# Kernel tuning notes

Measured on AMD Instinct MI355X. Metric: run time of the kernel, lower is better.

The kernel has to match this reference:

```python
import jax, jax.numpy as jnp
import numpy as np

D = 128
K = 8
TEMPERATURE = 1.0
LN_EPS = 1e-5
NORM_EPS = 1e-12


def setup_inputs() -> dict:
    key = jax.random.key(0)
    ks = jax.random.split(key, 6)
    B = 262144
    global_prosody = jax.random.normal(ks[0], (B, D), dtype=jnp.float32)
    W = jax.random.normal(ks[1], (D, D), dtype=jnp.float32) / np.sqrt(D)
    b = jnp.zeros((D,), dtype=jnp.float32)
    gamma = jnp.ones((D,), dtype=jnp.float32)
    beta = jnp.zeros((D,), dtype=jnp.float32)
    # codebook initialized as rows of an orthonormal basis (SVD of random init)
    init = jax.random.normal(ks[2], (D, K), dtype=jnp.float32)
    U, _, _ = jnp.linalg.svd(init, full_matrices=False)
    codebook = U[:, :K].T  # (K, D)
    return {"global_prosody": global_prosody, "W": W, "b": b,
            "gamma": gamma, "beta": beta, "codebook": codebook}


def _l2norm(x, axis=-1):
    n = jnp.sqrt(jnp.sum(x * x, axis=axis, keepdims=True))
    return x / jnp.maximum(n, NORM_EPS)


def reference(global_prosody, W, b, gamma, beta, codebook):
    # proj: Linear + LayerNorm
    h = global_prosody @ W.T + b                      # (B, D)
    mu = jnp.mean(h, axis=-1, keepdims=True)
    var = jnp.var(h, axis=-1, keepdims=True)
    h = (h - mu) / jnp.sqrt(var + LN_EPS) * gamma + beta
    # cosine-sim logits
    h_norm = _l2norm(h)                               # (B, D)
    cb_norm = _l2norm(codebook)                       # (K, D)
    logits = (h_norm @ cb_norm.T) / TEMPERATURE       # (B, K)
    soft_assign = jax.nn.softmax(logits, axis=-1)
    hard_indices = jnp.argmax(logits, axis=-1)        # (B,)
    hard_assign = jax.nn.one_hot(hard_indices, K, dtype=jnp.float32)
    # straight-through assignment
    assign = hard_assign + soft_assign - jax.lax.stop_gradient(soft_assign)
    embedding = assign @ codebook                     # (B, D)
    return hard_indices, soft_assign, embedding, logits
```

## Files before the change

kernel.cpp:

```cpp
#include <hip/hip_runtime.h>
#include <math.h>

#define DD 128
#define KK 8
#define LN_EPS 1e-5f
#define NORM_EPS 1e-12f

typedef __attribute__((ext_vector_type(8))) short bf16x8;
typedef __attribute__((ext_vector_type(16))) float f32x16;
typedef unsigned int uint;
typedef unsigned short ushort;

#define G2B_OFF_F   (122880 / 4)
#define SCAL_OFF_F  (123904 / 4)

__device__ inline void split3(float x, uint& h, uint& m, uint& l) {
    uint u0 = __float_as_uint(x);
    uint rh = (u0 + 0x7FFFu + ((u0 >> 16) & 1u)) & 0xFFFF0000u;
    float xh = __uint_as_float(rh);
    float r1 = x - xh;
    uint u1 = __float_as_uint(r1);
    uint rm = (u1 + 0x7FFFu + ((u1 >> 16) & 1u)) & 0xFFFF0000u;
    float xm = __uint_as_float(rm);
    float r2 = r1 - xm;
    uint u2 = __float_as_uint(r2);
    uint rl = (u2 + 0x7FFFu + ((u2 >> 16) & 1u));
    h = rh; m = rm; l = rl;
}

__device__ inline void split3t(float x, uint& h, uint& m, uint& l) {
    uint u0 = __float_as_uint(x);
    float xh = __uint_as_float(u0 & 0xFFFF0000u);
    float r1 = x - xh;
    uint u1 = __float_as_uint(r1);
    float xm = __uint_as_float(u1 & 0xFFFF0000u);
    float r2 = r1 - xm;
    h = u0; m = u1; l = __float_as_uint(r2);
}

__device__ inline uint packhi(uint a1, uint a0) {
    return __builtin_amdgcn_perm(a1, a0, 0x07060302u);
}

__device__ inline void split2packt(float e0, float e1, uint& ph, uint& pm, uint& pl) {
    uint h0, m0, l0, h1, m1, l1;
    split3t(e0, h0, m0, l0);
    split3t(e1, h1, m1, l1);
    ph = packhi(h1, h0);
    pm = packhi(m1, m0);
    pl = packhi(l1, l0);
}

union FragU  { uint4 u; bf16x8 f; };
union AccU16 { f32x16 v; float a[16]; };

__global__ void l1q_prep(const float* __restrict__ W, const float* __restrict__ b,
                         const float* __restrict__ gamma, const float* __restrict__ beta,
                         const float* __restrict__ cb, ushort* __restrict__ wsA,
                         float* __restrict__ ws)
{
    __shared__ float invn_s[KK];
    __shared__ float we[11][DD];
    __shared__ float wext[32][16];
    const int t = threadIdx.x;
    const int jt = blockIdx.x >> 3;
    const int ks = blockIdx.x & 7;

    if (jt == 4) {
        if (t < KK) {
            float s = 0.f;
            for (int j = 0; j < DD; ++j) { float v = cb[t * DD + j]; s = fmaf(v, v, s); }
            invn_s[t] = 1.0f / fmaxf(sqrtf(s), NORM_EPS);
        }
        __syncthreads();
        for (int idx = t; idx < 11 * DD; idx += 256) {
            int e = idx / DD, j = idx % DD;
            float g = gamma[j];
            float v;
            if (e == 0)      v = 1.0f;
            else if (e == 1) v = g * g;
            else if (e == 2) v = g * beta[j];
            else             v = cb[(e - 3) * DD + j] * invn_s[e - 3] * g;
            we[e][j] = v;
        }
        __syncthreads();

        if (ks == 0) {
            if (t < DD) {
                float g = gamma[t];
                float* g2b = ws + G2B_OFF_F;
                g2b[2 * t]     = g * g;
                g2b[2 * t + 1] = b[t];
            }
            float* scal = ws + SCAL_OFF_F;
            if (t < KK) {
                float in = invn_s[t];
                float p = 0.f, q = 0.f, cu = 0.f;
                for (int j = 0; j < DD; ++j) {
                    float c = cb[t * DD + j] * in;
                    p  = fmaf(c, gamma[j], p);
                    q  = fmaf(c, beta[j], q);
                    cu = fmaf(c * gamma[j], b[j], cu);
                }
                scal[t]      = p;
                scal[8 + t]  = q;
                scal[22 + t] = cu;
            }
            if (t == 16) { float s = 0.f; for (int j = 0; j < DD; ++j) { float g = gamma[j]; s = fmaf(g, g, s); } scal[16] = s; }
            if (t == 17) { float s = 0.f; for (int j = 0; j < DD; ++j) s = fmaf(gamma[j], beta[j], s); scal[17] = s; }
            if (t == 18) { float s = 0.f; for (int j = 0; j < DD; ++j) { float v = beta[j]; s = fmaf(v, v, s); } scal[18] = s; }
            if (t == 19) { float s = 0.f; for (int j = 0; j < DD; ++j) s += b[j]; scal[19] = s; }
            if (t == 20) { float s = 0.f; for (int j = 0; j < DD; ++j) s = fmaf(gamma[j] * gamma[j], b[j], s); scal[20] = s; }
            if (t == 21) { float s = 0.f; for (int j = 0; j < DD; ++j) s = fmaf(gamma[j] * beta[j], b[j], s); scal[21] = s; }
        }
    }

    for (int idx = t; idx < 512; idx += 256) {
        int jl = idx >> 4, kk = idx & 15;
        int k = ks * 16 + kk;
        float val;
        if (jt < 4) {
            val = W[(jt * 32 + jl) * DD + k];
        } else if (jl < 11) {
            float s = 0.f;
            for (int j = 0; j < DD; ++j) s = fmaf(we[jl][j], W[j * DD + k], s);
            val = s;
        } else {
            val = 0.f;
        }
        wext[jl][kk] = val;
    }
    __syncthreads();

    for (int idx = t; idx < 512; idx += 256) {
        int jl = idx >> 4, kk = idx & 15;
        int lane = jl + 32 * (kk >> 3);
        int i = kk & 7;
        uint h, m, l;
        split3(wext[jl][kk], h, m, l);
        int base = jt * 8 + ks;
        wsA[(0 * 40 + base) * 512 + lane * 8 + i] = (ushort)(h >> 16);
        wsA[(1 * 40 + base) * 512 + lane * 8 + i] = (ushort)(m >> 16);
        wsA[(2 * 40 + base) * 512 + lane * 8 + i] = (ushort)(l >> 16);
    }
}

__global__ __launch_bounds__(1024, 4)
void l1q_main(const float* __restrict__ x, const ushort* __restrict__ wsA,
              const float* __restrict__ wsf, const float* __restrict__ cb,
              float* __restrict__ out_idx, float* __restrict__ out_soft,
              float* __restrict__ out_emb, float* __restrict__ out_log,
              int B)
{
    __shared__ uint4 Wl4[7680];
    __shared__ float gath[16][352];
    __shared__ int   besti[16][32];
    __shared__ float g2b_s[256];
    __shared__ float scal_s[32];

    const int t = threadIdx.x;
    const int wave = t >> 6;
    const int lane = t & 63;
    const int n = lane & 31;
    const int h = lane >> 5;
    const int rowbase = blockIdx.x * 512 + wave * 32;
    const int row = rowbase + n;

    const float* xp = x + (size_t)row * DD + h * 8;
    float4 c0a = *(const float4*)(xp + 0);
    float4 c0c = *(const float4*)(xp + 4);
    float4 c1a = *(const float4*)(xp + 16);
    float4 c1c = *(const float4*)(xp + 20);

    {
        const uint4* src = (const uint4*)wsA;
        #pragma unroll
        for (int i = 0; i < 8; ++i) {
            int idx = t + i * 1024;
            if (idx < 7680) Wl4[idx] = src[idx];
        }
    }
    if (t < 256) g2b_s[t] = wsf[G2B_OFF_F + t];
    if (t < 32)  scal_s[t] = wsf[SCAL_OFF_F + t];
    __syncthreads();

    f32x16 acc[5];
    #pragma unroll
    for (int jt = 0; jt < 5; ++jt)
        #pragma unroll
        for (int r = 0; r < 16; ++r) acc[jt][r] = 0.f;

    #pragma unroll
    for (int ks = 0; ks < 8; ++ks) {
        int kp = (ks < 6) ? ks + 2 : 7;
        float4 pa = *(const float4*)(xp + kp * 16 + 0);
        float4 pc = *(const float4*)(xp + kp * 16 + 4);

        FragU xh, xm, xl;
        split2packt(c0a.x, c0a.y, xh.u.x, xm.u.x, xl.u.x);
        split2packt(c0a.z, c0a.w, xh.u.y, xm.u.y, xl.u.y);
        split2packt(c0c.x, c0c.y, xh.u.z, xm.u.z, xl.u.z);
        split2packt(c0c.z, c0c.w, xh.u.w, xm.u.w, xl.u.w);

        #pragma unroll
        for (int jt = 0; jt < 5; ++jt) {
            const int pl = jt * 8 + ks;
            FragU wh, wm, wl;
            wh.u = Wl4[(0 * 40 + pl) * 64 + lane];
            wm.u = Wl4[(1 * 40 + pl) * 64 + lane];
            wl.u = Wl4[(2 * 40 + pl) * 64 + lane];
            f32x16 c = acc[jt];
            c = __builtin_amdgcn_mfma_f32_32x32x16_bf16(wl.f, xh.f, c, 0, 0, 0);
            c = __builtin_amdgcn_mfma_f32_32x32x16_bf16(wh.f, xl.f, c, 0, 0, 0);
            c = __builtin_amdgcn_mfma_f32_32x32x16_bf16(wm.f, xm.f, c, 0, 0, 0);
            c = __builtin_amdgcn_mfma_f32_32x32x16_bf16(wm.f, xh.f, c, 0, 0, 0);
            c = __builtin_amdgcn_mfma_f32_32x32x16_bf16(wh.f, xm.f, c, 0, 0, 0);
            c = __builtin_amdgcn_mfma_f32_32x32x16_bf16(wh.f, xh.f, c, 0, 0, 0);
            acc[jt] = c;
        }
        c0a = c1a; c0c = c1c;
        c1a = pa;  c1c = pc;
    }

    float s2a = 0.f, t2a = 0.f;
    #pragma unroll
    for (int jt = 0; jt < 4; ++jt) {
        AccU16 a; a.v = acc[jt];
        #pragma unroll
        for (int rq = 0; rq < 4; ++rq) {
            int jb = jt * 32 + 8 * rq + 4 * h;
            #pragma unroll
            for (int r = 0; r < 4; ++r) {
                float2 gb = *(const float2*)&g2b_s[2 * (jb + r)];
                float hv = a.a[rq * 4 + r] + gb.y;
                float h2 = hv * hv;
                s2a += h2;
                t2a = fmaf(gb.x, h2, t2a);
            }
        }
    }
    s2a += __shfl_xor(s2a, 32);
    t2a += __shfl_xor(t2a, 32);

    {
        AccU16 a; a.v = acc[4];
        #pragma unroll
        for (int rq = 0; rq < 4; ++rq) {
            #pragma unroll
            for (int r = 0; r < 4; ++r) {
                int local = r + 8 * rq + 4 * h;
                if (local < 11) gath[wave][n * 11 + local] = a.a[rq * 4 + r];
            }
        }
    }
    __builtin_amdgcn_s_waitcnt(0);
    const float* gp = &gath[wave][n * 11];

    const float inv128 = 1.0f / 128.0f;
    const float cg2s = scal_s[16], cgbs = scal_s[17], cb2s = scal_s[18];

    float s1  = gp[0] + scal_s[19];
    float t1  = gp[1] + scal_s[20];
    float r1v = gp[2] + scal_s[21];
    float u[KK];
    #pragma unroll
    for (int k = 0; k < KK; ++k) u[k] = gp[3 + k] + scal_s[22 + k];

    float mu = s1 * inv128;
    float var = fmaf(-mu, mu, s2a * inv128);
    float istd = 1.0f / sqrtf(var + LN_EPS);
    float nrm2 = istd * istd * (t2a - 2.f * mu * t1 + mu * mu * cg2s)
               + 2.f * istd * (r1v - mu * cgbs) + cb2s;
    float rinv = 1.0f / fmaxf(sqrtf(fmaxf(nrm2, 0.f)), NORM_EPS);

    float lg[KK];
    #pragma unroll
    for (int k = 0; k < KK; ++k)
        lg[k] = (istd * (u[k] - mu * scal_s[k]) + scal_s[8 + k]) * rinv;

    float mx = lg[0]; int bi = 0;
    #pragma unroll
    for (int k = 1; k < KK; ++k) if (lg[k] > mx) { mx = lg[k]; bi = k; }

    float ex[KK], se = 0.f;
    #pragma unroll
    for (int k = 0; k < KK; ++k) { ex[k] = expf(lg[k] - mx); se += ex[k]; }
    float rse = 1.0f / se;

    const int m = rowbase + n;
    if (h == 0) {
        out_idx[m] = (float)bi;
        besti[wave][n] = bi;
        *(float4*)&out_log[(size_t)m * KK]     = make_float4(lg[0], lg[1], lg[2], lg[3]);
        *(float4*)&out_log[(size_t)m * KK + 4] = make_float4(lg[4], lg[5], lg[6], lg[7]);
    } else {
        *(float4*)&out_soft[(size_t)m * KK]     = make_float4(ex[0] * rse, ex[1] * rse, ex[2] * rse, ex[3] * rse);
        *(float4*)&out_soft[(size_t)m * KK + 4] = make_float4(ex[4] * rse, ex[5] * rse, ex[6] * rse, ex[7] * rse);
    }

    __builtin_amdgcn_s_waitcnt(0);
    const float4* cb4 = (const float4*)cb;
    float4* eo = (float4*)out_emb;
    #pragma unroll
    for (int i = 0; i < 16; ++i) {
        int f4 = lane + 64 * i;
        int rl = f4 >> 5;
        int c  = f4 & 31;
        int k0 = besti[wave][rl];
        eo[(size_t)(rowbase + rl) * 32 + c] = cb4[k0 * 32 + c];
    }
}

extern "C" void kernel_launch(void* const* d_in, const int* in_sizes, int n_in,
                              void* d_out, int out_size, void* d_ws, size_t ws_size,
                              hipStream_t stream) {
    const float* x     = (const float*)d_in[0];
    const float* W     = (const float*)d_in[1];
    const float* b     = (const float*)d_in[2];
    const float* gamma = (const float*)d_in[3];
    const float* beta  = (const float*)d_in[4];
    const float* cb    = (const float*)d_in[5];
    const int B = in_sizes[0] / DD;

    float*  ws  = (float*)d_ws;
    ushort* wsA = (ushort*)d_ws;

    float* out    = (float*)d_out;
    float* o_idx  = out;
    float* o_soft = out + (size_t)B;
    float* o_emb  = out + (size_t)B * (1 + KK);
    float* o_log  = out + (size_t)B * (1 + KK + DD);

    hipLaunchKernelGGL(l1q_prep, dim3(40), dim3(256), 0, stream, W, b, gamma, beta, cb, wsA, ws);
    const int grid = B / 512;
    hipLaunchKernelGGL(l1q_main, dim3(grid), dim3(1024), 0, stream,
                       x, wsA, ws, cb, o_idx, o_soft, o_emb, o_log, B);
}
```

Before: 288.3 us.

## Process two 512-row chunks per block to amortize weight staging

Each block now handles 1024 rows in two sequential chunks, halving the grid. This amortizes the per-block LDS load of the split bf16 weight fragments and lets the tail of the first chunk's k-loop prefetch the next chunk's x. The waitcnt calls now wait only on LDS (lgkmcnt) instead of on everything, so outstanding global stores no longer stall the wave. In exchange there are fewer blocks (256) to spread across the GPU, which reduces parallelism and may leave compute units idle.

```diff
diff --git a/kernel.cpp b/kernel.cpp
--- a/kernel.cpp
+++ b/kernel.cpp
@@ -163,10 +163,8 @@
     const int lane = t & 63;
     const int n = lane & 31;
     const int h = lane >> 5;
-    const int rowbase = blockIdx.x * 512 + wave * 32;
-    const int row = rowbase + n;
-
-    const float* xp = x + (size_t)row * DD + h * 8;
+
+    const float* xp = x + (size_t)(blockIdx.x * 1024 + wave * 32 + n) * DD + h * 8;
     float4 c0a = *(const float4*)(xp + 0);
     float4 c0c = *(const float4*)(xp + 4);
     float4 c1a = *(const float4*)(xp + 16);
@@ -184,130 +182,140 @@
     if (t < 32)  scal_s[t] = wsf[SCAL_OFF_F + t];
     __syncthreads();
 
-    f32x16 acc[5];
-    #pragma unroll
-    for (int jt = 0; jt < 5; ++jt)
-        #pragma unroll
-        for (int r = 0; r < 16; ++r) acc[jt][r] = 0.f;
-
-    #pragma unroll
-    for (int ks = 0; ks < 8; ++ks) {
-        int kp = (ks < 6) ? ks + 2 : 7;
-        float4 pa = *(const float4*)(xp + kp * 16 + 0);
-        float4 pc = *(const float4*)(xp + kp * 16 + 4);
-
-        FragU xh, xm, xl;
-        split2packt(c0a.x, c0a.y, xh.u.x, xm.u.x, xl.u.x);
-        split2packt(c0a.z, c0a.w, xh.u.y, xm.u.y, xl.u.y);
-        split2packt(c0c.x, c0c.y, xh.u.z, xm.u.z, xl.u.z);
-        split2packt(c0c.z, c0c.w, xh.u.w, xm.u.w, xl.u.w);
-
-        #pragma unroll
-        for (int jt = 0; jt < 5; ++jt) {
-            const int pl = jt * 8 + ks;
-            FragU wh, wm, wl;
-            wh.u = Wl4[(0 * 40 + pl) * 64 + lane];
-            wm.u = Wl4[(1 * 40 + pl) * 64 + lane];
-            wl.u = Wl4[(2 * 40 + pl) * 64 + lane];
-            f32x16 c = acc[jt];
-            c = __builtin_amdgcn_mfma_f32_32x32x16_bf16(wl.f, xh.f, c, 0, 0, 0);
-            c = __builtin_amdgcn_mfma_f32_32x32x16_bf16(wh.f, xl.f, c, 0, 0, 0);
-            c = __builtin_amdgcn_mfma_f32_32x32x16_bf16(wm.f, xm.f, c, 0, 0, 0);
-            c = __builtin_amdgcn_mfma_f32_32x32x16_bf16(wm.f, xh.f, c, 0, 0, 0);
-            c = __builtin_amdgcn_mfma_f32_32x32x16_bf16(wh.f, xm.f, c, 0, 0, 0);
-            c = __builtin_amdgcn_mfma_f32_32x32x16_bf16(wh.f, xh.f, c, 0, 0, 0);
-            acc[jt] = c;
-        }
-        c0a = c1a; c0c = c1c;
-        c1a = pa;  c1c = pc;
-    }
-
-    float s2a = 0.f, t2a = 0.f;
-    #pragma unroll
-    for (int jt = 0; jt < 4; ++jt) {
-        AccU16 a; a.v = acc[jt];
-        #pragma unroll
-        for (int rq = 0; rq < 4; ++rq) {
-            int jb = jt * 32 + 8 * rq + 4 * h;
+    const float inv128 = 1.0f / 128.0f;
+
+    #pragma unroll 1
+    for (int c = 0; c < 2; ++c) {
+        const int rowbase = blockIdx.x * 1024 + c * 512 + wave * 32;
+
+        f32x16 acc[5];
+        #pragma unroll
+        for (int jt = 0; jt < 5; ++jt)
             #pragma unroll
-            for (int r = 0; r < 4; ++r) {
-                float2 gb = *(const float2*)&g2b_s[2 * (jb + r)];
-                float hv = a.a[rq * 4 + r] + gb.y;
-                float h2 = hv * hv;
-                s2a += h2;
-                t2a = fmaf(gb.x, h2, t2a);
-            }
-        }
-    }
-    s2a += __shfl_xor(s2a, 32);
-    t2a += __shfl_xor(t2a, 32);
-
-    {
-        AccU16 a; a.v = acc[4];
-        #pragma unroll
-        for (int rq = 0; rq < 4; ++rq) {
+            for (int r = 0; r < 16; ++r) acc[jt][r] = 0.f;
+
+        #pragma unroll
+        for (int ks = 0; ks < 8; ++ks) {
+            const float* pf = (ks < 6) ? (xp + (ks + 2) * 16)
+                            : ((c == 0) ? (xp + 512 * DD + (ks - 6) * 16)
+                                        : (xp + 7 * 16));
+            float4 pa = *(const float4*)(pf + 0);
+            float4 pc = *(const float4*)(pf + 4);
+
+            FragU xh, xm, xl;
+            split2packt(c0a.x, c0a.y, xh.u.x, xm.u.x, xl.u.x);
+            split2packt(c0a.z, c0a.w, xh.u.y, xm.u.y, xl.u.y);
+            split2packt(c0c.x, c0c.y, xh.u.z, xm.u.z, xl.u.z);
+            split2packt(c0c.z, c0c.w, xh.u.w, xm.u.w, xl.u.w);
+
             #pragma unroll
-            for (int r = 0; r < 4; ++r) {
-                int local = r + 8 * rq + 4 * h;
-                if (local < 11) gath[wave][n * 11 + local] = a.a[rq * 4 + r];
-            }
-        }
-    }
-    __builtin_amdgcn_s_waitcnt(0);
-    const float* gp = &gath[wave][n * 11];
-
-    const float inv128 = 1.0f / 128.0f;
-    const float cg2s = scal_s[16], cgbs = scal_s[17], cb2s = scal_s[18];
-
-    float s1  = gp[0] + scal_s[19];
-    float t1  = gp[1] + scal_s[20];
-    float r1v = gp[2] + scal_s[21];
-    float u[KK];
-    #pragma unroll
-    for (int k = 0; k < KK; ++k) u[k] = gp[3 + k] + scal_s[22 + k];
-
-    float mu = s1 * inv128;
-    float var = fmaf(-mu, mu, s2a * inv128);
-    float istd = 1.0f / sqrtf(var + LN_EPS);
-    float nrm2 = istd * istd * (t2a - 2.f * mu * t1 + mu * mu * cg2s)
-               + 2.f * istd * (r1v - mu * cgbs) + cb2s;
-    float rinv = 1.0f / fmaxf(sqrtf(fmaxf(nrm2, 0.f)), NORM_EPS);
-
-    float lg[KK];
-    #pragma unroll
-    for (int k = 0; k < KK; ++k)
-        lg[k] = (istd * (u[k] - mu * scal_s[k]) + scal_s[8 + k]) * rinv;
-
-    float mx = lg[0]; int bi = 0;
-    #pragma unroll
-    for (int k = 1; k < KK; ++k) if (lg[k] > mx) { mx = lg[k]; bi = k; }
-
-    float ex[KK], se = 0.f;
-    #pragma unroll
-    for (int k = 0; k < KK; ++k) { ex[k] = expf(lg[k] - mx); se += ex[k]; }
-    float rse = 1.0f / se;
-
-    const int m = rowbase + n;
-    if (h == 0) {
-        out_idx[m] = (float)bi;
-        besti[wave][n] = bi;
-        *(float4*)&out_log[(size_t)m * KK]     = make_float4(lg[0], lg[1], lg[2], lg[3]);
-        *(float4*)&out_log[(size_t)m * KK + 4] = make_float4(lg[4], lg[5], lg[6], lg[7]);
-    } else {
-        *(float4*)&out_soft[(size_t)m * KK]     = make_float4(ex[0] * rse, ex[1] * rse, ex[2] * rse, ex[3] * rse);
-        *(float4*)&out_soft[(size_t)m * KK + 4] = make_float4(ex[4] * rse, ex[5] * rse, ex[6] * rse, ex[7] * rse);
-    }
-
-    __builtin_amdgcn_s_waitcnt(0);
-    const float4* cb4 = (const float4*)cb;
-    float4* eo = (float4*)out_emb;
-    #pragma unroll
-    for (int i = 0; i < 16; ++i) {
-        int f4 = lane + 64 * i;
-        int rl = f4 >> 5;
-        int c  = f4 & 31;
-        int k0 = besti[wave][rl];
-        eo[(size_t)(rowbase + rl) * 32 + c] = cb4[k0 * 32 + c];
+            for (int jt = 0; jt < 5; ++jt) {
+                const int pl = jt * 8 + ks;
+                FragU wh, wm, wl;
+                wh.u = Wl4[(0 * 40 + pl) * 64 + lane];
+                wm.u = Wl4[(1 * 40 + pl) * 64 + lane];
+                wl.u = Wl4[(2 * 40 + pl) * 64 + lane];
+                f32x16 cc = acc[jt];
+                cc = __builtin_amdgcn_mfma_f32_32x32x16_bf16(wl.f, xh.f, cc, 0, 0, 0);
+                cc = __builtin_amdgcn_mfma_f32_32x32x16_bf16(wh.f, xl.f, cc, 0, 0, 0);
+                cc = __builtin_amdgcn_mfma_f32_32x32x16_bf16(wm.f, xm.f, cc, 0, 0, 0);
+                cc = __builtin_amdgcn_mfma_f32_32x32x16_bf16(wm.f, xh.f, cc, 0, 0, 0);
+                cc = __builtin_amdgcn_mfma_f32_32x32x16_bf16(wh.f, xm.f, cc, 0, 0, 0);
+                cc = __builtin_amdgcn_mfma_f32_32x32x16_bf16(wh.f, xh.f, cc, 0, 0, 0);
+                acc[jt] = cc;
+            }
+            c0a = c1a; c0c = c1c;
+            c1a = pa;  c1c = pc;
+        }
+
+        float s2a = 0.f, t2a = 0.f;
+        #pragma unroll
+        for (int jt = 0; jt < 4; ++jt) {
+            AccU16 a; a.v = acc[jt];
+            #pragma unroll
+            for (int rq = 0; rq < 4; ++rq) {
+                int jb = jt * 32 + 8 * rq + 4 * h;
+                #pragma unroll
+                for (int r = 0; r < 4; ++r) {
+                    float2 gb = *(const float2*)&g2b_s[2 * (jb + r)];
+                    float hv = a.a[rq * 4 + r] + gb.y;
+                    float h2 = hv * hv;
+                    s2a += h2;
+                    t2a = fmaf(gb.x, h2, t2a);
+                }
+            }
+        }
+        s2a += __shfl_xor(s2a, 32);
+        t2a += __shfl_xor(t2a, 32);
+
+        {
+            AccU16 a; a.v = acc[4];
+            #pragma unroll
+            for (int rq = 0; rq < 4; ++rq) {
+                #pragma unroll
+                for (int r = 0; r < 4; ++r) {
+                    int local = r + 8 * rq + 4 * h;
+                    if (local < 11) gath[wave][n * 11 + local] = a.a[rq * 4 + r];
+                }
+            }
+        }
+        __builtin_amdgcn_s_waitcnt(0xc07f);
+        const float* gp = &gath[wave][n * 11];
+
+        const float cg2s = scal_s[16], cgbs = scal_s[17], cb2s = scal_s[18];
+
+        float s1  = gp[0] + scal_s[19];
+        float t1  = gp[1] + scal_s[20];
+        float r1v = gp[2] + scal_s[21];
+        float u[KK];
+        #pragma unroll
+        for (int k = 0; k < KK; ++k) u[k] = gp[3 + k] + scal_s[22 + k];
+
+        float mu = s1 * inv128;
+        float var = fmaf(-mu, mu, s2a * inv128);
+        float istd = 1.0f / sqrtf(var + LN_EPS);
+        float nrm2 = istd * istd * (t2a - 2.f * mu * t1 + mu * mu * cg2s)
+                   + 2.f * istd * (r1v - mu * cgbs) + cb2s;
+        float rinv = 1.0f / fmaxf(sqrtf(fmaxf(nrm2, 0.f)), NORM_EPS);
+
+        float lg[KK];
+        #pragma unroll
+        for (int k = 0; k < KK; ++k)
+            lg[k] = (istd * (u[k] - mu * scal_s[k]) + scal_s[8 + k]) * rinv;
+
+        float mx = lg[0]; int bi = 0;
+        #pragma unroll
+        for (int k = 1; k < KK; ++k) if (lg[k] > mx) { mx = lg[k]; bi = k; }
+
+        float ex[KK], se = 0.f;
+        #pragma unroll
+        for (int k = 0; k < KK; ++k) { ex[k] = expf(lg[k] - mx); se += ex[k]; }
+        float rse = 1.0f / se;
+
+        const int m = rowbase + n;
+        if (h == 0) {
+            out_idx[m] = (float)bi;
+            besti[wave][n] = bi;
+            *(float4*)&out_log[(size_t)m * KK]     = make_float4(lg[0], lg[1], lg[2], lg[3]);
+            *(float4*)&out_log[(size_t)m * KK + 4] = make_float4(lg[4], lg[5], lg[6], lg[7]);
+        } else {
+            *(float4*)&out_soft[(size_t)m * KK]     = make_float4(ex[0] * rse, ex[1] * rse, ex[2] * rse, ex[3] * rse);
+            *(float4*)&out_soft[(size_t)m * KK + 4] = make_float4(ex[4] * rse, ex[5] * rse, ex[6] * rse, ex[7] * rse);
+        }
+
+        __builtin_amdgcn_s_waitcnt(0xc07f);
+        const float4* cb4 = (const float4*)cb;
+        float4* eo = (float4*)out_emb;
+        #pragma unroll
+        for (int i = 0; i < 16; ++i) {
+            int f4 = lane + 64 * i;
+            int rl = f4 >> 5;
+            int cc = f4 & 31;
+            int k0 = besti[wave][rl];
+            eo[(size_t)(rowbase + rl) * 32 + cc] = cb4[k0 * 32 + cc];
+        }
+
+        xp += 512 * DD;
     }
 }
 
@@ -332,7 +340,7 @@
     float* o_log  = out + (size_t)B * (1 + KK + DD);
 
     hipLaunchKernelGGL(l1q_prep, dim3(40), dim3(256), 0, stream, W, b, gamma, beta, cb, wsA, ws);
-    const int grid = B / 512;
+    const int grid = B / 1024;
     hipLaunchKernelGGL(l1q_main, dim3(grid), dim3(1024), 0, stream,
                        x, wsA, ws, cb, o_idx, o_soft, o_emb, o_log, B);
 }
```

Result: slower. 297.7 us (+3.3%).

## Halve block size and stream low-limb and fifth-tile weights from global memory

Applied to the files above, without the earlier changes.

Blocks shrink from 1024 to 512 threads, each covering 256 rows. The shared-memory weight staging drops from 120 KB to 64 KB by keeping only the high and mid limbs of the first four column tiles in LDS. The low limb of those tiles and all three limbs of the fifth tile are instead read per k-step from global memory (L2-resident), prefetched one step ahead in registers. This is meant to lower LDS footprint and staging cost so more blocks fit per CU, at the price of more VGPRs and extra global loads inside the MFMA loop.

```diff
diff --git a/kernel.cpp b/kernel.cpp
--- a/kernel.cpp
+++ b/kernel.cpp
@@ -145,16 +145,16 @@
     }
 }
 
-__global__ __launch_bounds__(1024, 4)
+__global__ __launch_bounds__(512, 4)
 void l1q_main(const float* __restrict__ x, const ushort* __restrict__ wsA,
               const float* __restrict__ wsf, const float* __restrict__ cb,
               float* __restrict__ out_idx, float* __restrict__ out_soft,
               float* __restrict__ out_emb, float* __restrict__ out_log,
               int B)
 {
-    __shared__ uint4 Wl4[7680];
-    __shared__ float gath[16][352];
-    __shared__ int   besti[16][32];
+    __shared__ uint4 Wl4[4096];
+    __shared__ float gath[8][352];
+    __shared__ int   besti[8][32];
     __shared__ float g2b_s[256];
     __shared__ float scal_s[32];
 
@@ -163,7 +163,7 @@
     const int lane = t & 63;
     const int n = lane & 31;
     const int h = lane >> 5;
-    const int rowbase = blockIdx.x * 512 + wave * 32;
+    const int rowbase = blockIdx.x * 256 + wave * 32;
     const int row = rowbase + n;
 
     const float* xp = x + (size_t)row * DD + h * 8;
@@ -172,13 +172,21 @@
     float4 c1a = *(const float4*)(xp + 16);
     float4 c1c = *(const float4*)(xp + 20);
 
-    {
-        const uint4* src = (const uint4*)wsA;
-        #pragma unroll
-        for (int i = 0; i < 8; ++i) {
-            int idx = t + i * 1024;
-            if (idx < 7680) Wl4[idx] = src[idx];
-        }
+    const uint4* gW = (const uint4*)wsA;
+    FragU wl0, wl1, wl2, wl3, h4, m4, l4;
+    wl0.u = gW[(80 + 0 * 8 + 0) * 64 + lane];
+    wl1.u = gW[(80 + 1 * 8 + 0) * 64 + lane];
+    wl2.u = gW[(80 + 2 * 8 + 0) * 64 + lane];
+    wl3.u = gW[(80 + 3 * 8 + 0) * 64 + lane];
+    h4.u  = gW[(32 + 0) * 64 + lane];
+    m4.u  = gW[(72 + 0) * 64 + lane];
+    l4.u  = gW[(112 + 0) * 64 + lane];
+
+    #pragma unroll
+    for (int i = 0; i < 8; ++i) {
+        int idx = t + i * 512;
+        int limb = idx >> 11, rem = idx & 2047;
+        Wl4[idx] = gW[limb * 2560 + rem];
     }
     if (t < 256) g2b_s[t] = wsf[G2B_OFF_F + t];
     if (t < 32)  scal_s[t] = wsf[SCAL_OFF_F + t];
@@ -195,6 +203,16 @@
         int kp = (ks < 6) ? ks + 2 : 7;
         float4 pa = *(const float4*)(xp + kp * 16 + 0);
         float4 pc = *(const float4*)(xp + kp * 16 + 4);
+
+        int kn = (ks < 7) ? ks + 1 : 7;
+        FragU nl0, nl1, nl2, nl3, nh4, nm4, nl4;
+        nl0.u = gW[(80 + 0 * 8 + kn) * 64 + lane];
+        nl1.u = gW[(80 + 1 * 8 + kn) * 64 + lane];
+        nl2.u = gW[(80 + 2 * 8 + kn) * 64 + lane];
+        nl3.u = gW[(80 + 3 * 8 + kn) * 64 + lane];
+        nh4.u = gW[(32 + kn) * 64 + lane];
+        nm4.u = gW[(72 + kn) * 64 + lane];
+        nl4.u = gW[(112 + kn) * 64 + lane];
 
         FragU xh, xm, xl;
         split2packt(c0a.x, c0a.y, xh.u.x, xm.u.x, xl.u.x);
@@ -203,12 +221,12 @@
         split2packt(c0c.z, c0c.w, xh.u.w, xm.u.w, xl.u.w);
 
         #pragma unroll
-        for (int jt = 0; jt < 5; ++jt) {
+        for (int jt = 0; jt < 4; ++jt) {
             const int pl = jt * 8 + ks;
-            FragU wh, wm, wl;
-            wh.u = Wl4[(0 * 40 + pl) * 64 + lane];
-            wm.u = Wl4[(1 * 40 + pl) * 64 + lane];
-            wl.u = Wl4[(2 * 40 + pl) * 64 + lane];
+            FragU wh, wm;
+            wh.u = Wl4[pl * 64 + lane];
+            wm.u = Wl4[(32 + pl) * 64 + lane];
+            FragU wl = (jt == 0) ? wl0 : (jt == 1) ? wl1 : (jt == 2) ? wl2 : wl3;
             f32x16 c = acc[jt];
             c = __builtin_amdgcn_mfma_f32_32x32x16_bf16(wl.f, xh.f, c, 0, 0, 0);
             c = __builtin_amdgcn_mfma_f32_32x32x16_bf16(wh.f, xl.f, c, 0, 0, 0);
@@ -218,8 +236,21 @@
             c = __builtin_amdgcn_mfma_f32_32x32x16_bf16(wh.f, xh.f, c, 0, 0, 0);
             acc[jt] = c;
         }
+        {
+            f32x16 c = acc[4];
+            c = __builtin_amdgcn_mfma_f32_32x32x16_bf16(l4.f, xh.f, c, 0, 0, 0);
+            c = __builtin_amdgcn_mfma_f32_32x32x16_bf16(h4.f, xl.f, c, 0, 0, 0);
+            c = __builtin_amdgcn_mfma_f32_32x32x16_bf16(m4.f, xm.f, c, 0, 0, 0);
+            c = __builtin_amdgcn_mfma_f32_32x32x16_bf16(m4.f, xh.f, c, 0, 0, 0);
+            c = __builtin_amdgcn_mfma_f32_32x32x16_bf16(h4.f, xm.f, c, 0, 0, 0);
+            c = __builtin_amdgcn_mfma_f32_32x32x16_bf16(h4.f, xh.f, c, 0, 0, 0);
+            acc[4] = c;
+        }
+
         c0a = c1a; c0c = c1c;
         c1a = pa;  c1c = pc;
+        wl0 = nl0; wl1 = nl1; wl2 = nl2; wl3 = nl3;
+        h4 = nh4;  m4 = nm4;  l4 = nl4;
     }
 
     float s2a = 0.f, t2a = 0.f;
@@ -332,7 +363,7 @@
     float* o_log  = out + (size_t)B * (1 + KK + DD);
 
     hipLaunchKernelGGL(l1q_prep, dim3(40), dim3(256), 0, stream, W, b, gamma, beta, cb, wsA, ws);
-    const int grid = B / 512;
-    hipLaunchKernelGGL(l1q_main, dim3(grid), dim3(1024), 0, stream,
+    const int grid = B / 256;
+    hipLaunchKernelGGL(l1q_main, dim3(grid), dim3(512), 0, stream,
                        x, wsA, ws, cb, o_idx, o_soft, o_emb, o_log, B);
 }
```

Measured after the change: 452.2 us. 56.9% more time.
